# Kernel optimization log

Measured on AMD Instinct MI355X. Metric: run time of the kernel, lower is better.

## Reference

```python
import jax, jax.numpy as jnp
import numpy as np

N_NODES = 50000
N_EDGES = 1200000
N_REL = 45
IN_C, HID_C, OUT_C = 64, 32, 16


def setup_inputs() -> dict:
    key = jax.random.key(0)
    ks = jax.random.split(key, 9)
    x = jax.random.normal(ks[0], (N_NODES, IN_C), dtype=jnp.float32)
    edge_index = jax.random.randint(ks[1], (2, N_EDGES), 0, N_NODES, dtype=jnp.int64)
    edge_type = jax.random.randint(ks[2], (N_EDGES,), 0, N_REL, dtype=jnp.int64)
    s = 0.05
    W1 = jax.random.normal(ks[3], (N_REL, IN_C, HID_C), dtype=jnp.float32) * s
    root1 = jax.random.normal(ks[4], (IN_C, HID_C), dtype=jnp.float32) * s
    b1 = jax.random.normal(ks[5], (HID_C,), dtype=jnp.float32) * s
    W2 = jax.random.normal(ks[6], (N_REL, HID_C, OUT_C), dtype=jnp.float32) * s
    root2 = jax.random.normal(ks[7], (HID_C, OUT_C), dtype=jnp.float32) * s
    b2 = jax.random.normal(ks[8], (OUT_C,), dtype=jnp.float32) * s
    return {"x": x, "edge_index": edge_index, "edge_type": edge_type,
            "W1": W1, "root1": root1, "b1": b1,
            "W2": W2, "root2": root2, "b2": b2}


def rgcn_conv(x, edge_index, edge_type, W, root, b):
    # PyG RGCNConv: out_i = x_i @ root + b + sum_r mean_{j in N_r(i)} (x_j @ W_r)
    N = x.shape[0]
    R = W.shape[0]
    src, dst = edge_index[0], edge_index[1]
    # per-relation transform of all nodes: [R, N, out]
    h = jnp.einsum('ni,rio->rno', x, W)
    # per-edge message: gather transformed src feature for edge's relation
    msg = h[edge_type, src]                      # [E, out]
    # segment id combines (relation, dst) for per-relation mean aggregation
    seg = edge_type * N + dst                    # [E]
    sums = jax.ops.segment_sum(msg, seg, num_segments=R * N)        # [R*N, out]
    cnt = jax.ops.segment_sum(jnp.ones((msg.shape[0],), x.dtype), seg,
                              num_segments=R * N)                   # [R*N]
    mean = sums / jnp.maximum(cnt, 1.0)[:, None]
    agg = mean.reshape(R, N, -1).sum(axis=0)     # sum over relations -> [N, out]
    return agg + x @ root + b


def reference(x, edge_index, edge_type, W1, root1, b1, W2, root2, b2):
    h = rgcn_conv(x, edge_index, edge_type, W1, root1, b1)
    h = jax.nn.relu(h)
    out = rgcn_conv(h, edge_index, edge_type, W2, root2, b2)
    return out
```

## Files before the change

### kernel.cpp

```cpp
#include <hip/hip_runtime.h>
#include <hip/hip_fp16.h>
#include <cstdint>
#include <cstddef>

#define NN   50000
#define NE   1200000
#define NR   45
#define INC  64
#define HIDC 32
#define OUTC 16
#define MAXE 1202880
#define NCHUNK (MAXE/64)
#define EPB 4096
#define NB  ((NE + EPB - 1) / EPB)
#define QDW 3125
#define QDD 6250
#define NTILE ((NN + 255) / 256)
#define MS1 34
#define MS2 18

typedef _Float16 f16x8 __attribute__((ext_vector_type(8)));
typedef float    f32x4 __attribute__((ext_vector_type(4)));

union F16Bits { unsigned short u; _Float16 f; };
union ABFrag   { uint4 u; f16x8 f; };

__global__ __launch_bounds__(256) void preph_k(const float* __restrict__ W1,
                                               const float* __restrict__ W2,
                                               const float* __restrict__ x,
                                               const int* __restrict__ ei,
                                               const int* __restrict__ et,
                                               __half* __restrict__ W1f,
                                               __half* __restrict__ W2f,
                                               __half* __restrict__ xh,
                                               unsigned* __restrict__ ghist,
                                               unsigned* __restrict__ rsorted,
                                               unsigned* __restrict__ flagbuf) {
    __shared__ unsigned lh[NR];
    int t = threadIdx.x, b = blockIdx.x;
    if (t < NR) lh[t] = 0;
    __syncthreads();
    if (b < NB) {
        #pragma unroll
        for (int it = 0; it < EPB / 256; ++it) {
            int e = b * EPB + it * 256 + t;
            if (e < NE) {
                int r = et[e], src = ei[e], dst = ei[NE + e];
                if ((unsigned)r < NR && (unsigned)src < NN && (unsigned)dst < NN)
                    atomicAdd(&lh[r], 1u);
            }
        }
    }
    __syncthreads();
    if (b < NB && t < NR) ghist[b * NR + t] = lh[t];
    int g = b * 256 + t;
    int gthreads = gridDim.x * 256;
    for (int i = g; i < MAXE; i += gthreads) rsorted[i] = 0xFFFFFFFFu;
    if (b == 0) flagbuf[t] = 0;
    if (g < NR * 2048) {
        int r = g >> 11, rem = g & 2047;
        int kb = rem >> 10, nb = (rem >> 9) & 1;
        int lane = (rem >> 3) & 63, j = rem & 7;
        int k = kb * 32 + (lane >> 4) * 8 + j;
        int n = nb * 16 + (lane & 15);
        W1f[g] = __float2half(W1[(r * INC + k) * HIDC + n]);
    }
    if (g < NR * 512) {
        int r = g >> 9, rem = g & 511;
        int lane = (rem >> 3) & 63, j = rem & 7;
        int k = (lane >> 4) * 8 + j;
        int n = lane & 15;
        W2f[g] = __float2half(W2[(r * HIDC + k) * OUTC + n]);
    }
    if (g < NN * INC / 2) {
        float2 f = ((const float2*)x)[g];
        union { __half2 h; unsigned u; } cv;
        cv.h = __floats2half2_rn(f.x, f.y);
        ((unsigned*)xh)[g] = cv.u;
    }
}

__global__ __launch_bounds__(1024) void scat_k(const int* __restrict__ ei,
                                               const int* __restrict__ et,
                                               const unsigned* __restrict__ ghist,
                                               unsigned* __restrict__ rngs,
                                               int* __restrict__ chunkrel,
                                               unsigned* __restrict__ rsorted) {
    __shared__ unsigned reltot[NR];
    __shared__ unsigned mypart[NR];
    __shared__ unsigned relbase[NR + 1];
    __shared__ unsigned lbase[NR], lcur[NR];
    int t = threadIdx.x, bx = blockIdx.x;
    if (t < NR) {
        unsigned total = 0, part = 0;
        for (int b = 0; b < NB; ++b) {
            if (b == bx) part = total;
            total += ghist[b * NR + t];
        }
        reltot[t] = total;
        mypart[t] = part;
        lcur[t] = 0;
    }
    __syncthreads();
    if (t == 0) {
        unsigned acc = 0;
        for (int r = 0; r < NR; ++r) {
            relbase[r] = acc;
            acc += ((reltot[r] + 63u) >> 6) << 6;
        }
        relbase[NR] = acc;
    }
    __syncthreads();
    if (t < NR) lbase[t] = relbase[t] + mypart[t];
    __syncthreads();
    #pragma unroll
    for (int it = 0; it < EPB / 1024; ++it) {
        int e = bx * EPB + it * 1024 + t;
        if (e < NE) {
            int r = et[e], src = ei[e], dst = ei[NE + e];
            if ((unsigned)r < NR && (unsigned)src < NN && (unsigned)dst < NN) {
                unsigned local = atomicAdd(&lcur[r], 1u);
                rsorted[lbase[r] + local] = (unsigned)src | ((unsigned)dst << 16);
            }
        }
    }
    if (bx == 0) {
        if (t < NR) {
            rngs[2 * t]     = relbase[t];
            rngs[2 * t + 1] = relbase[t] + reltot[t];
        }
        for (int c = t; c < NCHUNK; c += 1024) {
            unsigned pos = (unsigned)c << 6;
            int lo = 0, hi = NR - 1;
            while (lo < hi) {
                int mid = (lo + hi + 1) >> 1;
                if (relbase[mid] <= pos) lo = mid; else hi = mid - 1;
            }
            chunkrel[c] = lo;
        }
    }
}

__global__ __launch_bounds__(1024) void relcnt_k(const unsigned* __restrict__ rsorted,
                                                 const unsigned* __restrict__ rngs,
                                                 unsigned short* __restrict__ cnt16,
                                                 unsigned short* __restrict__ rank16) {
    __shared__ unsigned lds[QDW];
    int r = blockIdx.x >> 3, q = blockIdx.x & 7, t = threadIdx.x;
    unsigned base = rngs[2 * r], end = rngs[2 * r + 1];
    unsigned dlo = q * QDD, dhi = dlo + QDD;
    for (int w = t; w < QDW; w += 1024) lds[w] = 0;
    __syncthreads();
    for (unsigned s = base + t; s < end; s += 1024) {
        unsigned d = rsorted[s] >> 16;
        if (d >= dlo && d < dhi) {
            unsigned off = d - dlo;
            atomicAdd(&lds[off >> 1], (off & 1) ? 0x10000u : 1u);
        }
    }
    __syncthreads();
    unsigned* __restrict__ cp = (unsigned*)(cnt16 + (size_t)r * NN + dlo);
    for (int w = t; w < QDW; w += 1024) cp[w] = lds[w];
    __syncthreads();
    for (int w = t; w < QDW; w += 1024) lds[w] = 0;
    __syncthreads();
    for (unsigned s = base + t; s < end; s += 1024) {
        unsigned d = rsorted[s] >> 16;
        if (d >= dlo && d < dhi) {
            unsigned off = d - dlo;
            unsigned old = atomicAdd(&lds[off >> 1], (off & 1) ? 0x10000u : 1u);
            rank16[s] = (unsigned short)((off & 1) ? (old >> 16) : (old & 0xFFFFu));
        }
    }
}

__global__ __launch_bounds__(256) void dp_k(const unsigned short* __restrict__ cnt16,
                                            unsigned* __restrict__ packed,
                                            unsigned* __restrict__ rowptr,
                                            unsigned* __restrict__ flags) {
    __shared__ unsigned wsum[4];
    __shared__ unsigned excl_s;
    int t = threadIdx.x, b = blockIdx.x;
    int lane = t & 63, wv = t >> 6;
    int dst = b * 256 + t;
    unsigned deg = 0;
    if (dst < NN) {
        unsigned run = 0;
        #pragma unroll 5
        for (int r = 0; r < NR; ++r) {
            unsigned c = cnt16[(size_t)r * NN + dst];
            F16Bits fb; fb.f = (_Float16)(c ? 1.0f / (float)c : 0.0f);
            packed[(size_t)r * NN + dst] = (run & 0xFFFFu) | ((unsigned)fb.u << 16);
            run += c;
        }
        deg = run;
    }
    unsigned s = deg;
    #pragma unroll
    for (int off = 1; off < 64; off <<= 1) {
        unsigned n = __shfl_up(s, off);
        if (lane >= off) s += n;
    }
    if (lane == 63) wsum[wv] = s;
    __syncthreads();
    unsigned waveoff = 0;
    if (wv > 0) waveoff += wsum[0];
    if (wv > 1) waveoff += wsum[1];
    if (wv > 2) waveoff += wsum[2];
    unsigned blockT = wsum[0] + wsum[1] + wsum[2] + wsum[3];
    unsigned local_excl = waveoff + s - deg;
    if (t == 0) {
        if (b == 0) {
            excl_s = 0;
            atomicExch(&flags[0], 0x80000000u | blockT);
        } else {
            atomicExch(&flags[b], 0x40000000u | blockT);
            unsigned ex = 0;
            int p = b - 1;
            while (p >= 0) {
                unsigned f = atomicAdd(&flags[p], 0u);
                unsigned st = f >> 30;
                if (st == 0) continue;
                ex += f & 0x3FFFFFFFu;
                if (st >= 2) break;
                --p;
            }
            excl_s = ex;
            atomicExch(&flags[b], 0x80000000u | (ex + blockT));
        }
    }
    __syncthreads();
    unsigned ex = excl_s;
    if (dst < NN) rowptr[dst] = ex + local_excl;
    if (b == (int)gridDim.x - 1 && t == 0) rowptr[NN] = ex + blockT;
}

__global__ __launch_bounds__(256) void finalize_k(const unsigned* __restrict__ rsorted,
                                                  const unsigned short* __restrict__ rank16,
                                                  const unsigned* __restrict__ packed,
                                                  const unsigned* __restrict__ rowptr,
                                                  const int* __restrict__ chunkrel,
                                                  uint2* __restrict__ pedges) {
    int s = blockIdx.x * 256 + threadIdx.x;
    if (s >= MAXE) return;
    unsigned v = rsorted[s];
    unsigned dst = v >> 16;
    if (dst >= NN) { pedges[s] = make_uint2(0u, 0x80000000u); return; }
    int r = chunkrel[s >> 6];
    unsigned pk = packed[(size_t)r * NN + dst];
    unsigned dpos = rowptr[dst] + (pk & 0xFFFFu) + (unsigned)rank16[s];
    pedges[s] = make_uint2((v & 0xFFFFu) | (pk & 0xFFFF0000u),
                           dpos | ((unsigned)r << 25));
}

__global__ __launch_bounds__(256) void msg1_k(const __half* __restrict__ xh,
                                              const __half* __restrict__ W1f,
                                              const uint2* __restrict__ pedges,
                                              __half* __restrict__ msg) {
    __shared__ float lmsg[4 * 16 * MS1];
    int tid = threadIdx.x;
    int wv = tid >> 6, lane = tid & 63;
    int wave = (blockIdx.x * 256 + tid) >> 6;
    if (wave >= NCHUNK) return;
    int e = (wave << 6) + lane;
    uint2 er = pedges[e];
    int w1 = (int)er.y;
    int rel = __builtin_amdgcn_readfirstlane((w1 >> 25) & 63);
    F16Bits fb; fb.u = (unsigned short)(er.x >> 16);
    float sc = (float)fb.f;
    int src = er.x & 0xFFFF;
    int drow = (w1 < 0) ? NE : (w1 & 0x1FFFFFF);
    const uint4* __restrict__ wf = (const uint4*)W1f + (size_t)rel * 256;
    ABFrag b00, b01, b10, b11;
    b00.u = wf[0 * 64 + lane];
    b01.u = wf[1 * 64 + lane];
    b10.u = wf[2 * 64 + lane];
    b11.u = wf[3 * 64 + lane];
    int quad = lane >> 4, col = lane & 15;
    float* __restrict__ lwave = lmsg + wv * (16 * MS1);
    #pragma unroll
    for (int tl = 0; tl < 4; ++tl) {
        int s = __shfl(src, tl * 16 + col);
        const uint4* __restrict__ xp = (const uint4*)(xh + (size_t)s * INC) + quad;
        ABFrag a0, a1;
        a0.u = xp[0];
        a1.u = xp[4];
        f32x4 acc0 = {0.f, 0.f, 0.f, 0.f}, acc1 = {0.f, 0.f, 0.f, 0.f};
        acc0 = __builtin_amdgcn_mfma_f32_16x16x32_f16(a0.f, b00.f, acc0, 0, 0, 0);
        acc0 = __builtin_amdgcn_mfma_f32_16x16x32_f16(a1.f, b10.f, acc0, 0, 0, 0);
        acc1 = __builtin_amdgcn_mfma_f32_16x16x32_f16(a0.f, b01.f, acc1, 0, 0, 0);
        acc1 = __builtin_amdgcn_mfma_f32_16x16x32_f16(a1.f, b11.f, acc1, 0, 0, 0);
        float* __restrict__ lt = lwave + (quad * 4) * MS1;
        #pragma unroll
        for (int i = 0; i < 4; ++i) {
            lt[i * MS1 + col]      = acc0[i];
            lt[i * MS1 + col + 16] = acc1[i];
        }
        if ((lane >> 4) == tl) {
            const float* __restrict__ myrow = lwave + (lane & 15) * MS1;
            unsigned um[16];
            #pragma unroll
            for (int k = 0; k < 16; ++k) {
                float2 vv = *(const float2*)(myrow + 2 * k);
                union { __half2 h; unsigned u; } cv;
                cv.h = __floats2half2_rn(vv.x * sc, vv.y * sc);
                um[k] = cv.u;
            }
            uint4* __restrict__ mrow = (uint4*)(msg + (size_t)drow * HIDC);
            #pragma unroll
            for (int q = 0; q < 4; ++q)
                mrow[q] = make_uint4(um[4*q], um[4*q+1], um[4*q+2], um[4*q+3]);
        }
    }
}

__global__ __launch_bounds__(256) void msg2_k(const __half* __restrict__ hh,
                                              const __half* __restrict__ W2f,
                                              const uint2* __restrict__ pedges,
                                              __half* __restrict__ msg) {
    __shared__ float lmsg[4 * 16 * MS2];
    int tid = threadIdx.x;
    int wv = tid >> 6, lane = tid & 63;
    int wave = (blockIdx.x * 256 + tid) >> 6;
    if (wave >= NCHUNK) return;
    int e = (wave << 6) + lane;
    uint2 er = pedges[e];
    int w1 = (int)er.y;
    int rel = __builtin_amdgcn_readfirstlane((w1 >> 25) & 63);
    F16Bits fb; fb.u = (unsigned short)(er.x >> 16);
    float sc = (float)fb.f;
    int src = er.x & 0xFFFF;
    int drow = (w1 < 0) ? NE : (w1 & 0x1FFFFFF);
    ABFrag bf;
    bf.u = ((const uint4*)W2f + (size_t)rel * 64)[lane];
    int quad = lane >> 4, col = lane & 15;
    float* __restrict__ lwave = lmsg + wv * (16 * MS2);
    #pragma unroll
    for (int tl = 0; tl < 4; ++tl) {
        int s = __shfl(src, tl * 16 + col);
        ABFrag a;
        a.u = *((const uint4*)(hh + (size_t)s * HIDC) + quad);
        f32x4 acc = {0.f, 0.f, 0.f, 0.f};
        acc = __builtin_amdgcn_mfma_f32_16x16x32_f16(a.f, bf.f, acc, 0, 0, 0);
        float* __restrict__ lt = lwave + (quad * 4) * MS2;
        #pragma unroll
        for (int i = 0; i < 4; ++i) lt[i * MS2 + col] = acc[i];
        if ((lane >> 4) == tl) {
            const float* __restrict__ myrow = lwave + (lane & 15) * MS2;
            unsigned um[8];
            #pragma unroll
            for (int k = 0; k < 8; ++k) {
                float2 vv = *(const float2*)(myrow + 2 * k);
                union { __half2 h; unsigned u; } cv;
                cv.h = __floats2half2_rn(vv.x * sc, vv.y * sc);
                um[k] = cv.u;
            }
            uint4* __restrict__ mrow = (uint4*)(msg + (size_t)drow * OUTC);
            mrow[0] = make_uint4(um[0], um[1], um[2], um[3]);
            mrow[1] = make_uint4(um[4], um[5], um[6], um[7]);
        }
    }
}

__global__ __launch_bounds__(256) void gather1_k(const float* __restrict__ x,
                                                 const float* __restrict__ root1,
                                                 const float* __restrict__ b1,
                                                 const __half* __restrict__ msg,
                                                 const unsigned* __restrict__ rowptr,
                                                 __half* __restrict__ hh) {
    __shared__ float sr[INC * HIDC];
    for (int k = threadIdx.x; k < INC * HIDC; k += 256) sr[k] = root1[k];
    __syncthreads();
    int wid = (blockIdx.x * 256 + threadIdx.x) >> 6;
    int lane = threadIdx.x & 63;
    int c2 = lane & 15, sub = lane >> 4;
    unsigned k0 = rowptr[wid], k1 = rowptr[wid + 1];
    float accx = 0.f, accy = 0.f;
    for (unsigned k = k0 + sub; k < k1; k += 4) {
        union { __half2 hh2; unsigned u; } cv;
        cv.u = ((const unsigned*)(msg + (size_t)k * HIDC))[c2];
        float2 f = __half22float2(cv.hh2);
        accx += f.x; accy += f.y;
    }
    const float4* __restrict__ xp = (const float4*)(x + (size_t)wid * INC + sub * 16);
    #pragma unroll
    for (int q = 0; q < 4; ++q) {
        float4 xr = xp[q];
        const float* xs = (const float*)&xr;
        #pragma unroll
        for (int j = 0; j < 4; ++j) {
            int in = sub * 16 + q * 4 + j;
            float2 rt = *(const float2*)&sr[in * HIDC + 2 * c2];
            accx = fmaf(xs[j], rt.x, accx);
            accy = fmaf(xs[j], rt.y, accy);
        }
    }
    accx += __shfl_xor(accx, 16); accy += __shfl_xor(accy, 16);
    accx += __shfl_xor(accx, 32); accy += __shfl_xor(accy, 32);
    if (sub == 0) {
        float2 bb = *(const float2*)&b1[2 * c2];
        float vx = accx + bb.x, vy = accy + bb.y;
        union { __half2 h2; unsigned u; } cv;
        cv.h2 = __floats2half2_rn(vx > 0.f ? vx : 0.f, vy > 0.f ? vy : 0.f);
        ((unsigned*)hh)[(size_t)wid * (HIDC / 2) + c2] = cv.u;
    }
}

__global__ __launch_bounds__(256) void gather2_k(const __half* __restrict__ hh,
                                                 const float* __restrict__ root2,
                                                 const float* __restrict__ b2,
                                                 const __half* __restrict__ msg,
                                                 const unsigned* __restrict__ rowptr,
                                                 float* __restrict__ out) {
    __shared__ float sr[HIDC * OUTC];
    for (int k = threadIdx.x; k < HIDC * OUTC; k += 256) sr[k] = root2[k];
    __syncthreads();
    int wid = (blockIdx.x * 256 + threadIdx.x) >> 6;
    int lane = threadIdx.x & 63;
    int c2 = lane & 7, sub = lane >> 3;
    unsigned k0 = rowptr[wid], k1 = rowptr[wid + 1];
    float accx = 0.f, accy = 0.f;
    for (unsigned k = k0 + sub; k < k1; k += 8) {
        union { __half2 hh2; unsigned u; } cv;
        cv.u = ((const unsigned*)(msg + (size_t)k * OUTC))[c2];
        float2 f = __half22float2(cv.hh2);
        accx += f.x; accy += f.y;
    }
    uint2 hw = *(const uint2*)(hh + (size_t)wid * HIDC + sub * 4);
    union { __half2 h2; unsigned u; } ca, cb;
    ca.u = hw.x; cb.u = hw.y;
    float2 ha = __half22float2(ca.h2), hb = __half22float2(cb.h2);
    float hs[4] = { ha.x, ha.y, hb.x, hb.y };
    #pragma unroll
    for (int j = 0; j < 4; ++j) {
        int in = sub * 4 + j;
        float2 rt = *(const float2*)&sr[in * OUTC + 2 * c2];
        accx = fmaf(hs[j], rt.x, accx);
        accy = fmaf(hs[j], rt.y, accy);
    }
    accx += __shfl_xor(accx, 8);  accy += __shfl_xor(accy, 8);
    accx += __shfl_xor(accx, 16); accy += __shfl_xor(accy, 16);
    accx += __shfl_xor(accx, 32); accy += __shfl_xor(accy, 32);
    if (sub == 0) {
        float2 bb = *(const float2*)&b2[2 * c2];
        *(float2*)&out[(size_t)wid * OUTC + 2 * c2] =
            make_float2(accx + bb.x, accy + bb.y);
    }
}

extern "C" void kernel_launch(void* const* d_in, const int* in_sizes, int n_in,
                              void* d_out, int out_size, void* d_ws, size_t ws_size,
                              hipStream_t stream) {
    const float* x     = (const float*)d_in[0];
    const int*   ei    = (const int*)d_in[1];
    const int*   et    = (const int*)d_in[2];
    const float* W1    = (const float*)d_in[3];
    const float* root1 = (const float*)d_in[4];
    const float* b1    = (const float*)d_in[5];
    const float* W2    = (const float*)d_in[6];
    const float* root2 = (const float*)d_in[7];
    const float* b2    = (const float*)d_in[8];
    float* out = (float*)d_out;

    char* ws = (char*)d_ws;
    size_t o = 0;
    auto alloc = [&](size_t bytes) -> char* {
        char* p = ws + o;
        o = (o + bytes + 255) & ~(size_t)255;
        return p;
    };
    unsigned* rsorted = (unsigned*)alloc((size_t)MAXE * 4);
    unsigned* flagbuf = (unsigned*)alloc(256 * 4);
    unsigned* ghist   = (unsigned*)alloc((size_t)NR * NB * 4);
    unsigned* rngs    = (unsigned*)alloc((size_t)NR * 2 * 4);
    int*      chunkrel= (int*)     alloc((size_t)NCHUNK * 4);
    unsigned short* rank16 = (unsigned short*)alloc((size_t)MAXE * 2);
    unsigned short* cnt16  = (unsigned short*)alloc((size_t)NR * NN * 2);
    unsigned* packed  = (unsigned*)alloc((size_t)NR * NN * 4);
    unsigned* rowptr  = (unsigned*)alloc(((size_t)NN + 1) * 4);
    uint2*    pedges  = (uint2*)   alloc((size_t)MAXE * 8);
    __half*   W1f     = (__half*)  alloc((size_t)NR * 2048 * 2);
    __half*   W2f     = (__half*)  alloc((size_t)NR * 512 * 2);
    __half*   xh      = (__half*)  alloc((size_t)NN * INC * 2);
    __half*   hh      = (__half*)  alloc((size_t)NN * HIDC * 2);
    char*     msgraw  = alloc(((size_t)NE + 1) * 64);
    __half*   msg1    = (__half*)msgraw;
    __half*   msg2    = (__half*)msgraw;

    int prep_grid = NN * INC / 2 / 256;
    preph_k   <<<prep_grid, 256, 0, stream>>>(W1, W2, x, ei, et, W1f, W2f, xh,
                                              ghist, rsorted, flagbuf);
    scat_k    <<<NB, 1024, 0, stream>>>(ei, et, ghist, rngs, chunkrel, rsorted);
    relcnt_k  <<<8 * NR, 1024, 0, stream>>>(rsorted, rngs, cnt16, rank16);
    dp_k      <<<NTILE, 256, 0, stream>>>(cnt16, packed, rowptr, flagbuf + 32);
    finalize_k<<<(MAXE + 255) / 256, 256, 0, stream>>>(rsorted, rank16, packed,
                                                       rowptr, chunkrel, pedges);
    msg1_k    <<<(MAXE + 255) / 256, 256, 0, stream>>>(xh, W1f, pedges, msg1);
    gather1_k <<<NN * 64 / 256, 256, 0, stream>>>(x, root1, b1, msg1, rowptr, hh);
    msg2_k    <<<(MAXE + 255) / 256, 256, 0, stream>>>(hh, W2f, pedges, msg2);
    gather2_k <<<NN * 64 / 256, 256, 0, stream>>>(hh, root2, b2, msg2, rowptr, out);
}
```

Baseline: 326.1 us.

## Write MFMA outputs directly with interleaved channel layout; single-pass relation count

The message kernels no longer stage MFMA accumulators through LDS and transpose them; each lane writes its result directly with shuffles for the destination row and scale. Because the stored message channels then come out interleaved, W2 is permuted and the gather kernels' root and bias indexing is adjusted to match. The gathers of source rows are also hoisted so all loads issue before the MFMAs. relcnt_k now covers half the nodes per block with a larger LDS array and fuses the count and rank passes into one, so rsorted is read once, at the cost of fewer blocks and more LDS per block. The direct stores become narrow 4-byte scattered writes instead of 16-byte row writes.

```diff
diff --git a/kernel.cpp b/kernel.cpp
--- a/kernel.cpp
+++ b/kernel.cpp
@@ -13,11 +13,10 @@
 #define NCHUNK (MAXE/64)
 #define EPB 4096
 #define NB  ((NE + EPB - 1) / EPB)
-#define QDW 3125
-#define QDD 6250
+#define QDW2 12500
+#define QDD2 25000
 #define NTILE ((NN + 255) / 256)
-#define MS1 34
-#define MS2 18
+
 
 typedef _Float16 f16x8 __attribute__((ext_vector_type(8)));
 typedef float    f32x4 __attribute__((ext_vector_type(4)));
@@ -69,8 +68,9 @@
         int r = g >> 9, rem = g & 511;
         int lane = (rem >> 3) & 63, j = rem & 7;
         int k = (lane >> 4) * 8 + j;
+        int kc = (k >> 1) + ((k & 1) << 4);
         int n = lane & 15;
-        W2f[g] = __float2half(W2[(r * HIDC + k) * OUTC + n]);
+        W2f[g] = __float2half(W2[(r * HIDC + kc) * OUTC + n]);
     }
     if (g < NN * INC / 2) {
         float2 f = ((const float2*)x)[g];
@@ -145,24 +145,11 @@
                                                  const unsigned* __restrict__ rngs,
                                                  unsigned short* __restrict__ cnt16,
                                                  unsigned short* __restrict__ rank16) {
-    __shared__ unsigned lds[QDW];
-    int r = blockIdx.x >> 3, q = blockIdx.x & 7, t = threadIdx.x;
+    __shared__ unsigned lds[QDW2];
+    int r = blockIdx.x >> 1, q = blockIdx.x & 1, t = threadIdx.x;
     unsigned base = rngs[2 * r], end = rngs[2 * r + 1];
-    unsigned dlo = q * QDD, dhi = dlo + QDD;
-    for (int w = t; w < QDW; w += 1024) lds[w] = 0;
-    __syncthreads();
-    for (unsigned s = base + t; s < end; s += 1024) {
-        unsigned d = rsorted[s] >> 16;
-        if (d >= dlo && d < dhi) {
-            unsigned off = d - dlo;
-            atomicAdd(&lds[off >> 1], (off & 1) ? 0x10000u : 1u);
-        }
-    }
-    __syncthreads();
-    unsigned* __restrict__ cp = (unsigned*)(cnt16 + (size_t)r * NN + dlo);
-    for (int w = t; w < QDW; w += 1024) cp[w] = lds[w];
-    __syncthreads();
-    for (int w = t; w < QDW; w += 1024) lds[w] = 0;
+    unsigned dlo = q * QDD2, dhi = dlo + QDD2;
+    for (int w = t; w < QDW2; w += 1024) lds[w] = 0;
     __syncthreads();
     for (unsigned s = base + t; s < end; s += 1024) {
         unsigned d = rsorted[s] >> 16;
@@ -172,6 +159,9 @@
             rank16[s] = (unsigned short)((off & 1) ? (old >> 16) : (old & 0xFFFFu));
         }
     }
+    __syncthreads();
+    unsigned* __restrict__ cp = (unsigned*)(cnt16 + (size_t)r * NN + dlo);
+    for (int w = t; w < QDW2; w += 1024) cp[w] = lds[w];
 }
 
 __global__ __launch_bounds__(256) void dp_k(const unsigned short* __restrict__ cnt16,
@@ -257,9 +247,8 @@
                                               const __half* __restrict__ W1f,
                                               const uint2* __restrict__ pedges,
                                               __half* __restrict__ msg) {
-    __shared__ float lmsg[4 * 16 * MS1];
     int tid = threadIdx.x;
-    int wv = tid >> 6, lane = tid & 63;
+    int lane = tid & 63;
     int wave = (blockIdx.x * 256 + tid) >> 6;
     if (wave >= NCHUNK) return;
     int e = (wave << 6) + lane;
@@ -277,39 +266,29 @@
     b10.u = wf[2 * 64 + lane];
     b11.u = wf[3 * 64 + lane];
     int quad = lane >> 4, col = lane & 15;
-    float* __restrict__ lwave = lmsg + wv * (16 * MS1);
+    ABFrag a0[4], a1[4];
     #pragma unroll
     for (int tl = 0; tl < 4; ++tl) {
         int s = __shfl(src, tl * 16 + col);
         const uint4* __restrict__ xp = (const uint4*)(xh + (size_t)s * INC) + quad;
-        ABFrag a0, a1;
-        a0.u = xp[0];
-        a1.u = xp[4];
+        a0[tl].u = xp[0];
+        a1[tl].u = xp[4];
+    }
+    #pragma unroll
+    for (int tl = 0; tl < 4; ++tl) {
         f32x4 acc0 = {0.f, 0.f, 0.f, 0.f}, acc1 = {0.f, 0.f, 0.f, 0.f};
-        acc0 = __builtin_amdgcn_mfma_f32_16x16x32_f16(a0.f, b00.f, acc0, 0, 0, 0);
-        acc0 = __builtin_amdgcn_mfma_f32_16x16x32_f16(a1.f, b10.f, acc0, 0, 0, 0);
-        acc1 = __builtin_amdgcn_mfma_f32_16x16x32_f16(a0.f, b01.f, acc1, 0, 0, 0);
-        acc1 = __builtin_amdgcn_mfma_f32_16x16x32_f16(a1.f, b11.f, acc1, 0, 0, 0);
-        float* __restrict__ lt = lwave + (quad * 4) * MS1;
+        acc0 = __builtin_amdgcn_mfma_f32_16x16x32_f16(a0[tl].f, b00.f, acc0, 0, 0, 0);
+        acc0 = __builtin_amdgcn_mfma_f32_16x16x32_f16(a1[tl].f, b10.f, acc0, 0, 0, 0);
+        acc1 = __builtin_amdgcn_mfma_f32_16x16x32_f16(a0[tl].f, b01.f, acc1, 0, 0, 0);
+        acc1 = __builtin_amdgcn_mfma_f32_16x16x32_f16(a1[tl].f, b11.f, acc1, 0, 0, 0);
         #pragma unroll
         for (int i = 0; i < 4; ++i) {
-            lt[i * MS1 + col]      = acc0[i];
-            lt[i * MS1 + col + 16] = acc1[i];
-        }
-        if ((lane >> 4) == tl) {
-            const float* __restrict__ myrow = lwave + (lane & 15) * MS1;
-            unsigned um[16];
-            #pragma unroll
-            for (int k = 0; k < 16; ++k) {
-                float2 vv = *(const float2*)(myrow + 2 * k);
-                union { __half2 h; unsigned u; } cv;
-                cv.h = __floats2half2_rn(vv.x * sc, vv.y * sc);
-                um[k] = cv.u;
-            }
-            uint4* __restrict__ mrow = (uint4*)(msg + (size_t)drow * HIDC);
-            #pragma unroll
-            for (int q = 0; q < 4; ++q)
-                mrow[q] = make_uint4(um[4*q], um[4*q+1], um[4*q+2], um[4*q+3]);
+            int ee = tl * 16 + quad * 4 + i;
+            int dr   = __shfl(drow, ee);
+            float si = __shfl(sc, ee);
+            union { __half2 h; unsigned u; } cv;
+            cv.h = __floats2half2_rn(acc0[i] * si, acc1[i] * si);
+            ((unsigned*)(msg + (size_t)dr * HIDC))[col] = cv.u;
         }
     }
 }
@@ -318,9 +297,8 @@
                                               const __half* __restrict__ W2f,
                                               const uint2* __restrict__ pedges,
                                               __half* __restrict__ msg) {
-    __shared__ float lmsg[4 * 16 * MS2];
     int tid = threadIdx.x;
-    int wv = tid >> 6, lane = tid & 63;
+    int lane = tid & 63;
     int wave = (blockIdx.x * 256 + tid) >> 6;
     if (wave >= NCHUNK) return;
     int e = (wave << 6) + lane;
@@ -334,30 +312,28 @@
     ABFrag bf;
     bf.u = ((const uint4*)W2f + (size_t)rel * 64)[lane];
     int quad = lane >> 4, col = lane & 15;
-    float* __restrict__ lwave = lmsg + wv * (16 * MS2);
+    ABFrag a[4];
     #pragma unroll
     for (int tl = 0; tl < 4; ++tl) {
         int s = __shfl(src, tl * 16 + col);
-        ABFrag a;
-        a.u = *((const uint4*)(hh + (size_t)s * HIDC) + quad);
+        a[tl].u = *((const uint4*)(hh + (size_t)s * HIDC) + quad);
+    }
+    #pragma unroll
+    for (int tl = 0; tl < 4; ++tl) {
         f32x4 acc = {0.f, 0.f, 0.f, 0.f};
-        acc = __builtin_amdgcn_mfma_f32_16x16x32_f16(a.f, bf.f, acc, 0, 0, 0);
-        float* __restrict__ lt = lwave + (quad * 4) * MS2;
+        acc = __builtin_amdgcn_mfma_f32_16x16x32_f16(a[tl].f, bf.f, acc, 0, 0, 0);
         #pragma unroll
-        for (int i = 0; i < 4; ++i) lt[i * MS2 + col] = acc[i];
-        if ((lane >> 4) == tl) {
-            const float* __restrict__ myrow = lwave + (lane & 15) * MS2;
-            unsigned um[8];
-            #pragma unroll
-            for (int k = 0; k < 8; ++k) {
-                float2 vv = *(const float2*)(myrow + 2 * k);
+        for (int i = 0; i < 4; ++i) {
+            int ee = tl * 16 + quad * 4 + i;
+            int dr   = __shfl(drow, ee);
+            float si = __shfl(sc, ee);
+            float v  = acc[i] * si;
+            float p  = __shfl_xor(v, 8);
+            if (col < 8) {
                 union { __half2 h; unsigned u; } cv;
-                cv.h = __floats2half2_rn(vv.x * sc, vv.y * sc);
-                um[k] = cv.u;
+                cv.h = __floats2half2_rn(v, p);
+                ((unsigned*)(msg + (size_t)dr * OUTC))[col] = cv.u;
             }
-            uint4* __restrict__ mrow = (uint4*)(msg + (size_t)drow * OUTC);
-            mrow[0] = make_uint4(um[0], um[1], um[2], um[3]);
-            mrow[1] = make_uint4(um[4], um[5], um[6], um[7]);
         }
     }
 }
@@ -390,16 +366,14 @@
         #pragma unroll
         for (int j = 0; j < 4; ++j) {
             int in = sub * 16 + q * 4 + j;
-            float2 rt = *(const float2*)&sr[in * HIDC + 2 * c2];
-            accx = fmaf(xs[j], rt.x, accx);
-            accy = fmaf(xs[j], rt.y, accy);
+            accx = fmaf(xs[j], sr[in * HIDC + c2], accx);
+            accy = fmaf(xs[j], sr[in * HIDC + c2 + 16], accy);
         }
     }
     accx += __shfl_xor(accx, 16); accy += __shfl_xor(accy, 16);
     accx += __shfl_xor(accx, 32); accy += __shfl_xor(accy, 32);
     if (sub == 0) {
-        float2 bb = *(const float2*)&b1[2 * c2];
-        float vx = accx + bb.x, vy = accy + bb.y;
+        float vx = accx + b1[c2], vy = accy + b1[c2 + 16];
         union { __half2 h2; unsigned u; } cv;
         cv.h2 = __floats2half2_rn(vx > 0.f ? vx : 0.f, vy > 0.f ? vy : 0.f);
         ((unsigned*)hh)[(size_t)wid * (HIDC / 2) + c2] = cv.u;
@@ -433,18 +407,16 @@
     float hs[4] = { ha.x, ha.y, hb.x, hb.y };
     #pragma unroll
     for (int j = 0; j < 4; ++j) {
-        int in = sub * 4 + j;
-        float2 rt = *(const float2*)&sr[in * OUTC + 2 * c2];
-        accx = fmaf(hs[j], rt.x, accx);
-        accy = fmaf(hs[j], rt.y, accy);
+        int in = 2 * sub + (j >> 1) + ((j & 1) << 4);
+        accx = fmaf(hs[j], sr[in * OUTC + c2], accx);
+        accy = fmaf(hs[j], sr[in * OUTC + c2 + 8], accy);
     }
     accx += __shfl_xor(accx, 8);  accy += __shfl_xor(accy, 8);
     accx += __shfl_xor(accx, 16); accy += __shfl_xor(accy, 16);
     accx += __shfl_xor(accx, 32); accy += __shfl_xor(accy, 32);
     if (sub == 0) {
-        float2 bb = *(const float2*)&b2[2 * c2];
-        *(float2*)&out[(size_t)wid * OUTC + 2 * c2] =
-            make_float2(accx + bb.x, accy + bb.y);
+        out[(size_t)wid * OUTC + c2]     = accx + b2[c2];
+        out[(size_t)wid * OUTC + c2 + 8] = accy + b2[c2 + 8];
     }
 }
 
@@ -491,7 +463,7 @@
     preph_k   <<<prep_grid, 256, 0, stream>>>(W1, W2, x, ei, et, W1f, W2f, xh,
                                               ghist, rsorted, flagbuf);
     scat_k    <<<NB, 1024, 0, stream>>>(ei, et, ghist, rngs, chunkrel, rsorted);
-    relcnt_k  <<<8 * NR, 1024, 0, stream>>>(rsorted, rngs, cnt16, rank16);
+    relcnt_k  <<<2 * NR, 1024, 0, stream>>>(rsorted, rngs, cnt16, rank16);
     dp_k      <<<NTILE, 256, 0, stream>>>(cnt16, packed, rowptr, flagbuf + 32);
     finalize_k<<<(MAXE + 255) / 256, 256, 0, stream>>>(rsorted, rank16, packed,
                                                        rowptr, chunkrel, pedges);
```

After: 296.8 us. 1.1x faster.
